# Performance work log

Hardware: AMD Instinct MI355X
Metric: run time of the kernel (lower is better)

The kernel has to match this reference:

```python
import jax, jax.numpy as jnp
import numpy as np

GN_EPS = 1e-6
NUM_GROUPS = 32


def group_norm(x, gamma, beta):
    # x: [B,H,W,C], normalize per-sample over (H,W, C//G) within each of G groups
    B, H, W, C = x.shape
    G = NUM_GROUPS
    xg = x.reshape(B, H, W, G, C // G)
    mean = jnp.mean(xg, axis=(1, 2, 4), keepdims=True)
    var = jnp.var(xg, axis=(1, 2, 4), keepdims=True)
    xg = (xg - mean) * jax.lax.rsqrt(var + GN_EPS)
    x = xg.reshape(B, H, W, C)
    return x * gamma + beta


def setup_inputs() -> dict:
    key = jax.random.key(0)
    ks = jax.random.split(key, 6)
    B, H, W, C = 4, 64, 64, 512
    scale = 1.0 / np.sqrt(C)
    return {
        "x": jax.random.normal(ks[0], (B, H, W, C), jnp.float32),
        "gn_gamma": jnp.ones((C,), jnp.float32),
        "gn_beta": jnp.zeros((C,), jnp.float32),
        "Wq": jax.random.normal(ks[1], (C, C), jnp.float32) * scale,
        "bq": jnp.zeros((C,), jnp.float32),
        "Wk": jax.random.normal(ks[2], (C, C), jnp.float32) * scale,
        "bk": jnp.zeros((C,), jnp.float32),
        "Wv": jax.random.normal(ks[3], (C, C), jnp.float32) * scale,
        "bv": jnp.zeros((C,), jnp.float32),
        "Wo": jax.random.normal(ks[4], (C, C), jnp.float32) * scale,
        "bo": jnp.zeros((C,), jnp.float32),
    }


def reference(x, gn_gamma, gn_beta, Wq, bq, Wk, bk, Wv, bv, Wo, bo):
    B, H, W, C = x.shape
    h = group_norm(x, gn_gamma, gn_beta)          # [B,H,W,C]
    t = h.reshape(B, H * W, C)                     # flatten spatial tokens
    q = t @ Wq + bq                                # [B,N,C]
    k = t @ Wk + bk
    v = t @ Wv + bv
    scores = jnp.einsum('bnc,bmc->bnm', q, k) * (C ** -0.5)  # [B,N,N]
    attn = jax.nn.softmax(scores, axis=-1)
    out = jnp.einsum('bnm,bmc->bnc', attn, v)      # [B,N,C]
    out = out @ Wo + bo
    return out.reshape(B, H, W, C) + x
```

## Files before the change

kernel.cpp:

```cpp
#include <hip/hip_runtime.h>
#include <stdint.h>

using u16 = unsigned short;
typedef __attribute__((ext_vector_type(8))) short short8;
typedef __attribute__((ext_vector_type(4))) float floatx4;

__device__ __forceinline__ float b2f(u16 s) {
    union { unsigned u; float f; } x; x.u = ((unsigned)s) << 16; return x.f;
}
__device__ __forceinline__ u16 f2b(float f) {
    unsigned u = __float_as_uint(f);
    unsigned r = (u + 0x7fffu + ((u >> 16) & 1u)) >> 16;
    return (u16)r;
}

__device__ __forceinline__ void gl16(const u16* g, u16* l) {
    __builtin_amdgcn_global_load_lds((const __attribute__((address_space(1))) void*)g,
                                     (__attribute__((address_space(3))) void*)l,
                                     16, 0, 0);
}

__global__ __launch_bounds__(256) void gn_stats_k(const float* __restrict__ x,
                                                  float* __restrict__ part) {
    int bid = blockIdx.x;
    int bg = bid >> 2, pt = bid & 3;
    int b = bg >> 5, g = bg & 31;
    const size_t base = (size_t)b * 4096 * 512 + g * 16;
    int t = threadIdx.x;
    float s = 0.f, ss = 0.f;
    for (int it = 0; it < 16; ++it) {
        int vi = pt * 4096 + it * 256 + t;
        int n = vi >> 2;
        int j = (vi & 3) * 4;
        float4 u = *(const float4*)(x + base + (size_t)n * 512 + j);
        s += u.x + u.y + u.z + u.w;
        ss += u.x * u.x + u.y * u.y + u.z * u.z + u.w * u.w;
    }
    for (int off = 32; off; off >>= 1) {
        s  += __shfl_down(s, off, 64);
        ss += __shfl_down(ss, off, 64);
    }
    __shared__ float rs[4], rss[4];
    int lane = t & 63, w = t >> 6;
    if (lane == 0) { rs[w] = s; rss[w] = ss; }
    __syncthreads();
    if (t == 0) {
        part[bg * 8 + pt * 2]     = rs[0] + rs[1] + rs[2] + rs[3];
        part[bg * 8 + pt * 2 + 1] = rss[0] + rss[1] + rss[2] + rss[3];
    }
}

__global__ __launch_bounds__(256) void gn_apply_k(const float* __restrict__ x,
                                                  const float* __restrict__ gamma,
                                                  const float* __restrict__ beta,
                                                  const float* __restrict__ part,
                                                  u16* __restrict__ h) {
    size_t v = (size_t)blockIdx.x * 256 + threadIdx.x;
    size_t e = v * 4;
    int c = (int)(e & 511);
    int b = (int)(e >> 21);
    int g = c >> 4;
    int bg = b * 32 + g;
    float4 p0 = *(const float4*)(part + bg * 8);
    float4 p1 = *(const float4*)(part + bg * 8 + 4);
    float S1 = p0.x + p0.z + p1.x + p1.z;
    float S2 = p0.y + p0.w + p1.y + p1.w;
    float mean = S1 * (1.f / 65536.f);
    float var  = S2 * (1.f / 65536.f) - mean * mean;
    float rstd = rsqrtf(var + 1e-6f);
    float4 xv = *(const float4*)(x + e);
    float4 gv = *(const float4*)(gamma + c);
    float4 bv = *(const float4*)(beta + c);
    ushort4 o;
    o.x = f2b((xv.x - mean) * rstd * gv.x + bv.x);
    o.y = f2b((xv.y - mean) * rstd * gv.y + bv.y);
    o.z = f2b((xv.z - mean) * rstd * gv.z + bv.z);
    o.w = f2b((xv.w - mean) * rstd * gv.w + bv.w);
    *(ushort4*)(h + e) = o;
}

__global__ __launch_bounds__(256) void transpose_f2b4(const float* __restrict__ Wq,
                                                      const float* __restrict__ Wk,
                                                      const float* __restrict__ Wv,
                                                      const float* __restrict__ Wo,
                                                      u16* __restrict__ wqkv_t,
                                                      u16* __restrict__ wo_t) {
    int z = blockIdx.z;
    const float* src = (z == 0) ? Wq : (z == 1) ? Wk : (z == 2) ? Wv : Wo;
    u16* dst = (z < 3) ? wqkv_t + (size_t)z * 512 * 512 : wo_t;
    __shared__ float tile[32][33];
    int tx = threadIdx.x, ty = threadIdx.y;
    int r0 = blockIdx.x * 32, c0 = blockIdx.y * 32;
#pragma unroll
    for (int i = 0; i < 4; ++i)
        tile[ty + i * 8][tx] = src[(size_t)(r0 + ty + i * 8) * 512 + c0 + tx];
    __syncthreads();
#pragma unroll
    for (int i = 0; i < 4; ++i)
        dst[(size_t)(c0 + ty + i * 8) * 512 + r0 + tx] = f2b(tile[tx][ty + i * 8]);
}

__global__ __launch_bounds__(256) void concat_bias_f(const float* __restrict__ bq,
                                                     const float* __restrict__ bk,
                                                     const float* __restrict__ bv,
                                                     float* __restrict__ dst) {
    int i = blockIdx.x * 256 + threadIdx.x;
    const float* src = (i < 512) ? bq : (i < 1024) ? bk : bv;
    dst[i] = src[i & 511];
}

__global__ __launch_bounds__(256) void gemm_bt(const u16* __restrict__ A, int lda,
                                               const u16* __restrict__ B, int ldb,
                                               u16* __restrict__ C, float* __restrict__ Cf,
                                               int ldc,
                                               const float* __restrict__ bias,
                                               const float* __restrict__ resid,
                                               u16* __restrict__ Vt,
                                               int K, float scale) {
    __shared__ u16 As[128 * 32];
    __shared__ u16 Bs[128 * 32];
    const int t = threadIdx.x;
    const int lane = t & 63, w = t >> 6;
    const int wm = (w >> 1) * 64, wn = (w & 1) * 64;
    const int r = lane & 15, q = lane >> 4;
    const int m0 = blockIdx.x * 128;
    const int n0 = blockIdx.y * 128;

    floatx4 acc[4][4];
#pragma unroll
    for (int mi = 0; mi < 4; ++mi)
#pragma unroll
        for (int ni = 0; ni < 4; ++ni) acc[mi][ni] = (floatx4){0.f, 0.f, 0.f, 0.f};

    const int srow = lane >> 2;
    const int scol = (lane & 3) * 8;
    const u16* gA = A + (size_t)(m0 + w * 32 + srow) * lda + scol;
    const u16* gB = B + (size_t)(n0 + w * 32 + srow) * ldb + scol;
    u16* lA = As + w * 1024;
    u16* lB = Bs + w * 1024;

    for (int k0 = 0; k0 < K; k0 += 32) {
        __syncthreads();
        gl16(gA,                     lA);
        gl16(gA + (size_t)16 * lda,  lA + 512);
        gl16(gB,                     lB);
        gl16(gB + (size_t)16 * ldb,  lB + 512);
        gA += 32; gB += 32;
        __syncthreads();
        short8 af[4], bfr[4];
#pragma unroll
        for (int mi = 0; mi < 4; ++mi)
            af[mi] = *(const short8*)(As + (wm + mi * 16 + r) * 32 + q * 8);
#pragma unroll
        for (int ni = 0; ni < 4; ++ni)
            bfr[ni] = *(const short8*)(Bs + (wn + ni * 16 + r) * 32 + q * 8);
#pragma unroll
        for (int mi = 0; mi < 4; ++mi)
#pragma unroll
            for (int ni = 0; ni < 4; ++ni)
                acc[mi][ni] = __builtin_amdgcn_mfma_f32_16x16x32_bf16(af[mi], bfr[ni],
                                                                      acc[mi][ni], 0, 0, 0);
    }

    const bool vpath = (Vt != nullptr) && (n0 >= 1024);
#pragma unroll
    for (int ni = 0; ni < 4; ++ni) {
        int col = n0 + wn + ni * 16 + r;
        float bv = bias ? bias[col] : 0.f;
#pragma unroll
        for (int mi = 0; mi < 4; ++mi) {
            int rowb = m0 + wm + mi * 16 + q * 4;
            if (vpath) {
                int c = col - 1024;
                int b = rowb >> 12, n = rowb & 4095;
                ushort4 o;
                o.x = f2b(acc[mi][ni][0] * scale + bv);
                o.y = f2b(acc[mi][ni][1] * scale + bv);
                o.z = f2b(acc[mi][ni][2] * scale + bv);
                o.w = f2b(acc[mi][ni][3] * scale + bv);
                *(ushort4*)(Vt + (((size_t)b * 512 + c) << 12) + n) = o;
            } else {
#pragma unroll
                for (int i = 0; i < 4; ++i) {
                    size_t off = (size_t)(rowb + i) * ldc + col;
                    float v = acc[mi][ni][i] * scale + bv;
                    if (resid) v += resid[off];
                    if (Cf) Cf[off] = v;
                    else    C[off] = f2b(v);
                }
            }
        }
    }
}

#define FLASH_SMEM 147968
__global__ __launch_bounds__(512, 2) void flash_k(const u16* __restrict__ qkv,
                                                  const u16* __restrict__ vt,
                                                  u16* __restrict__ ao) {
    extern __shared__ u16 smem[];
    u16* Ks = smem;
    u16* Vs = smem + 32768;
    u16* Pl = smem + 65536;
    float* lex = (float*)(smem + 73728);
    const int t = threadIdx.x;
    const int lane = t & 63, w = t >> 6;
    const int rw = w & 3, kh = w >> 2;
    const int r = lane & 15, q = lane >> 4;
    const int swz = (q ^ ((r >> 1) & 3)) * 8;
    const int lin = blockIdx.y * 64 + blockIdx.x;
    const int xcd = lin & 7, slot = lin >> 3;
    const int b = xcd >> 1;
    const int qt = ((xcd & 1) << 5) | slot;
    const u16* qb = qkv + (size_t)b * 4096 * 1536;
    const u16* kb = qb + 512;
    const u16* vb = vt + (size_t)b * 512 * 4096;
    u16* aob = ao + (size_t)b * 4096 * 512;
    const int wch = w * 64;

    auto stageK = [&](int buf, int kt, int g) {
#pragma unroll
        for (int j = 0; j < 4; ++j) {
            int u = t + j * 512;
            int key = (u & 511) >> 2;
            int sub = u >> 9;
            int c = ((u & 3) ^ ((key >> 1) & 3)) * 8;
            gl16(kb + (size_t)(kt * 128 + key) * 1536 + g * 128 + sub * 32 + c,
                 Ks + buf * 16384 + u * 8);
        }
    };
    auto stageV = [&](int buf, int kt, int k) {
#pragma unroll
        for (int j = 0; j < 4; ++j) {
            int u = t + j * 512;
            int ch = u >> 2;
            int c = ((u & 3) ^ ((ch >> 1) & 3)) * 8;
            gl16(vb + (size_t)ch * 4096 + kt * 128 + k * 32 + c,
                 Vs + buf * 16384 + u * 8);
        }
    };

    stageK(0, 0, 0);
    stageV(0, 0, 0);

    const int qrow = qt * 64 + rw * 16 + r;
    short8 Qreg[16];
#pragma unroll
    for (int kit = 0; kit < 16; ++kit)
        Qreg[kit] = *(const short8*)(qb + (size_t)qrow * 1536 + kit * 32 + q * 8);

    floatx4 acc_o[16];
#pragma unroll
    for (int i = 0; i < 16; ++i) acc_o[i] = (floatx4){0.f, 0.f, 0.f, 0.f};
    float l_half = 0.f;
    const float sc2 = 0.06375872f;

    for (int kt = 0; kt < 32; ++kt) {
        floatx4 acc_s[4];
#pragma unroll
        for (int mi = 0; mi < 4; ++mi) acc_s[mi] = (floatx4){0.f, 0.f, 0.f, 0.f};
#pragma unroll
        for (int g = 0; g < 4; ++g) {
            __syncthreads();
            if (g < 3) stageK((g + 1) & 1, kt, g + 1);
            const u16* kbase = Ks + (g & 1) * 16384;
#pragma unroll
            for (int s = 0; s < 4; ++s) {
                const u16* sbase = kbase + s * 4096;
#pragma unroll
                for (int mi = 0; mi < 4; ++mi) {
                    short8 af = *(const short8*)(sbase + (kh * 64 + mi * 16 + r) * 32 + swz);
                    acc_s[mi] = __builtin_amdgcn_mfma_f32_16x16x32_bf16(
                        af, Qreg[g * 4 + s], acc_s[mi], 0, 0, 0);
                }
            }
        }
        float rs = 0.f;
#pragma unroll
        for (int mi = 0; mi < 4; ++mi)
#pragma unroll
            for (int i = 0; i < 4; ++i) {
                float pv = __builtin_amdgcn_exp2f(acc_s[mi][i] * sc2);
                acc_s[mi][i] = pv;
                rs += pv;
            }
        rs += __shfl_xor(rs, 16, 64);
        rs += __shfl_xor(rs, 32, 64);
        l_half += rs;
#pragma unroll
        for (int mi = 0; mi < 4; ++mi) {
            uint2 vv;
            vv.x = (unsigned)f2b(acc_s[mi][0]) | ((unsigned)f2b(acc_s[mi][1]) << 16);
            vv.y = (unsigned)f2b(acc_s[mi][2]) | ((unsigned)f2b(acc_s[mi][3]) << 16);
            *(uint2*)(Pl + (rw * 16 + r) * 128 +
                      (((kh * 8 + 2 * mi + (q >> 1)) ^ (r & 7)) * 8) + (q & 1) * 4) = vv;
        }
#pragma unroll
        for (int k = 0; k < 4; ++k) {
            __syncthreads();
            if (k < 3)        stageV((k + 1) & 1, kt, k + 1);
            else if (kt < 31) stageV(0, kt + 1, 0);
            if (k == 0 && kt < 31) stageK(0, kt + 1, 0);
            short8 ap[4];
#pragma unroll
            for (int mi = 0; mi < 4; ++mi)
                ap[mi] = *(const short8*)(Pl + (mi * 16 + r) * 128 +
                                          (((k * 4 + q) ^ (r & 7)) * 8));
            const u16* vbase = Vs + (k & 1) * 16384;
#pragma unroll
            for (int ni = 0; ni < 4; ++ni) {
                short8 bf = *(const short8*)(vbase + (wch + ni * 16 + r) * 32 + swz);
#pragma unroll
                for (int mi = 0; mi < 4; ++mi)
                    acc_o[mi * 4 + ni] = __builtin_amdgcn_mfma_f32_16x16x32_bf16(
                        ap[mi], bf, acc_o[mi * 4 + ni], 0, 0, 0);
            }
        }
    }
    if (q == 0) lex[w * 16 + r] = l_half;
    __syncthreads();
#pragma unroll
    for (int mi = 0; mi < 4; ++mi) {
        float4 la = *(const float4*)(lex + mi * 16 + q * 4);
        float4 lb = *(const float4*)(lex + 64 + mi * 16 + q * 4);
        float i0 = 1.f / (la.x + lb.x), i1 = 1.f / (la.y + lb.y);
        float i2 = 1.f / (la.z + lb.z), i3 = 1.f / (la.w + lb.w);
        int rowb = qt * 64 + mi * 16 + q * 4;
#pragma unroll
        for (int ni = 0; ni < 4; ++ni) {
            int col = wch + ni * 16 + r;
            aob[(size_t)(rowb + 0) * 512 + col] = f2b(acc_o[mi * 4 + ni][0] * i0);
            aob[(size_t)(rowb + 1) * 512 + col] = f2b(acc_o[mi * 4 + ni][1] * i1);
            aob[(size_t)(rowb + 2) * 512 + col] = f2b(acc_o[mi * 4 + ni][2] * i2);
            aob[(size_t)(rowb + 3) * 512 + col] = f2b(acc_o[mi * 4 + ni][3] * i3);
        }
    }
}

extern "C" void kernel_launch(void* const* d_in, const int* in_sizes, int n_in,
                              void* d_out, int out_size, void* d_ws, size_t ws_size,
                              hipStream_t stream) {
    const float* x     = (const float*)d_in[0];
    const float* gamma = (const float*)d_in[1];
    const float* beta  = (const float*)d_in[2];
    const float* Wq    = (const float*)d_in[3];
    const float* bq    = (const float*)d_in[4];
    const float* Wk    = (const float*)d_in[5];
    const float* bk    = (const float*)d_in[6];
    const float* Wv    = (const float*)d_in[7];
    const float* bv    = (const float*)d_in[8];
    const float* Wo    = (const float*)d_in[9];
    const float* bo    = (const float*)d_in[10];
    float* out = (float*)d_out;

    char* ws = (char*)d_ws;
    float* stats  = (float*)(ws);
    float* bqkv   = (float*)(ws + 4096);
    u16*   wqkv_t = (u16*)(ws + 16384);
    u16*   wo_t   = wqkv_t + (size_t)1536 * 512;
    u16*   h      = wo_t + (size_t)512 * 512;
    u16*   qkv    = h   + (size_t)16384 * 512;
    u16*   vt     = qkv + (size_t)16384 * 1536;
    u16*   ao     = h;

    dim3 tblk(32, 8, 1);
    transpose_f2b4<<<dim3(16, 16, 4), tblk, 0, stream>>>(Wq, Wk, Wv, Wo, wqkv_t, wo_t);
    concat_bias_f<<<6, 256, 0, stream>>>(bq, bk, bv, bqkv);

    gn_stats_k<<<512, 256, 0, stream>>>(x, stats);
    gn_apply_k<<<8192, 256, 0, stream>>>(x, gamma, beta, stats, h);

    gemm_bt<<<dim3(128, 12, 1), 256, 0, stream>>>(h, 512, wqkv_t, 512,
                                                  qkv, nullptr, 1536, bqkv, nullptr,
                                                  vt, 512, 1.0f);
    hipFuncSetAttribute((const void*)flash_k,
                        hipFuncAttributeMaxDynamicSharedMemorySize, FLASH_SMEM);
    flash_k<<<dim3(64, 4, 1), 512, FLASH_SMEM, stream>>>(qkv, vt, ao);

    gemm_bt<<<dim3(128, 4, 1), 256, 0, stream>>>(ao, 512, wo_t, 512,
                                                 nullptr, out, 512, bo, x,
                                                 nullptr, 512, 1.0f);
}
```

Before: 397.5 us.

## Double GEMM K-tile to 64 with XOR-swizzled LDS and drop flash XCD remap

The GEMM now stages a 64-wide K slice per iteration, using an XOR swizzle on the LDS column chunks to avoid bank conflicts. Each stage runs two MFMA sub-steps, which halves the number of barrier pairs per K. Separately, the flash kernel drops its XCD-aware block-to-(batch, q-tile) remap in favour of plain blockIdx mapping. That removal may reduce L2 locality of K/V per batch across XCDs.

```diff
diff --git a/kernel.cpp b/kernel.cpp
--- a/kernel.cpp
+++ b/kernel.cpp
@@ -117,8 +117,8 @@
                                                const float* __restrict__ resid,
                                                u16* __restrict__ Vt,
                                                int K, float scale) {
-    __shared__ u16 As[128 * 32];
-    __shared__ u16 Bs[128 * 32];
+    __shared__ u16 As[128 * 64];
+    __shared__ u16 Bs[128 * 64];
     const int t = threadIdx.x;
     const int lane = t & 63, w = t >> 6;
     const int wm = (w >> 1) * 64, wn = (w & 1) * 64;
@@ -132,34 +132,42 @@
 #pragma unroll
         for (int ni = 0; ni < 4; ++ni) acc[mi][ni] = (floatx4){0.f, 0.f, 0.f, 0.f};
 
-    const int srow = lane >> 2;
-    const int scol = (lane & 3) * 8;
-    const u16* gA = A + (size_t)(m0 + w * 32 + srow) * lda + scol;
-    const u16* gB = B + (size_t)(n0 + w * 32 + srow) * ldb + scol;
-    u16* lA = As + w * 1024;
-    u16* lB = Bs + w * 1024;
-
-    for (int k0 = 0; k0 < K; k0 += 32) {
+    int srow[4], soff[4];
+#pragma unroll
+    for (int j = 0; j < 4; ++j) {
+        int e = j * 2048 + t * 8;
+        srow[j] = e >> 6;
+        soff[j] = ((((e >> 3) & 7) ^ (srow[j] & 7)) * 8);
+    }
+    const int swzA = (r & 7);
+
+    for (int k0 = 0; k0 < K; k0 += 64) {
         __syncthreads();
-        gl16(gA,                     lA);
-        gl16(gA + (size_t)16 * lda,  lA + 512);
-        gl16(gB,                     lB);
-        gl16(gB + (size_t)16 * ldb,  lB + 512);
-        gA += 32; gB += 32;
+#pragma unroll
+        for (int j = 0; j < 4; ++j) {
+            int e = j * 2048 + t * 8;
+            gl16(A + (size_t)(m0 + srow[j]) * lda + k0 + soff[j], As + e);
+            gl16(B + (size_t)(n0 + srow[j]) * ldb + k0 + soff[j], Bs + e);
+        }
         __syncthreads();
-        short8 af[4], bfr[4];
-#pragma unroll
-        for (int mi = 0; mi < 4; ++mi)
-            af[mi] = *(const short8*)(As + (wm + mi * 16 + r) * 32 + q * 8);
-#pragma unroll
-        for (int ni = 0; ni < 4; ++ni)
-            bfr[ni] = *(const short8*)(Bs + (wn + ni * 16 + r) * 32 + q * 8);
-#pragma unroll
-        for (int mi = 0; mi < 4; ++mi)
+#pragma unroll
+        for (int kk = 0; kk < 2; ++kk) {
+            short8 af[4], bfr[4];
+#pragma unroll
+            for (int mi = 0; mi < 4; ++mi)
+                af[mi] = *(const short8*)(As + (wm + mi * 16 + r) * 64 +
+                                          (((kk * 4 + q) ^ swzA) * 8));
 #pragma unroll
             for (int ni = 0; ni < 4; ++ni)
-                acc[mi][ni] = __builtin_amdgcn_mfma_f32_16x16x32_bf16(af[mi], bfr[ni],
-                                                                      acc[mi][ni], 0, 0, 0);
+                bfr[ni] = *(const short8*)(Bs + (wn + ni * 16 + r) * 64 +
+                                           (((kk * 4 + q) ^ swzA) * 8));
+#pragma unroll
+            for (int mi = 0; mi < 4; ++mi)
+#pragma unroll
+                for (int ni = 0; ni < 4; ++ni)
+                    acc[mi][ni] = __builtin_amdgcn_mfma_f32_16x16x32_bf16(
+                        af[mi], bfr[ni], acc[mi][ni], 0, 0, 0);
+        }
     }
 
     const bool vpath = (Vt != nullptr) && (n0 >= 1024);
@@ -207,10 +215,7 @@
     const int rw = w & 3, kh = w >> 2;
     const int r = lane & 15, q = lane >> 4;
     const int swz = (q ^ ((r >> 1) & 3)) * 8;
-    const int lin = blockIdx.y * 64 + blockIdx.x;
-    const int xcd = lin & 7, slot = lin >> 3;
-    const int b = xcd >> 1;
-    const int qt = ((xcd & 1) << 5) | slot;
+    const int b = blockIdx.y, qt = blockIdx.x;
     const u16* qb = qkv + (size_t)b * 4096 * 1536;
     const u16* kb = qb + 512;
     const u16* vb = vt + (size_t)b * 512 * 4096;
```

Result: faster. 373.3 us (-6.1%).
